# Optimization experiments

Measured on AMD Instinct MI355X. Metric: run time of the kernel, lower is better.

The kernel has to match this reference:

```python
import jax, jax.numpy as jnp
import numpy as np

H, D, K, FF = 4, 256, 1024, 1024  # n_head, d_model, key_feature_dim, dim_feedforward
L, B = 2048, 4                    # pixels, batch


def setup_inputs() -> dict:
    key = jax.random.key(0)
    ks = jax.random.split(key, 12)
    def g(k, shape, s=0.02):
        return jax.random.normal(k, shape, jnp.float32) * s
    return dict(
        src=jax.random.normal(ks[0], (L, B, D), jnp.float32),
        WK=g(ks[1], (H, K, D), (2.0 / K) ** 0.5),
        WQ=g(ks[2], (H, K, D), (2.0 / K) ** 0.5),
        WV=g(ks[3], (H, D, D), (2.0 / D) ** 0.5),
        TC=g(ks[4], (H, D, D)),
        ENw1=g(ks[5], (H, FF, D)), ENb1=jnp.zeros((H, FF), jnp.float32),
        ENw2=g(ks[6], (H, D, FF)), ENb2=jnp.zeros((H, D), jnp.float32),
        ENg=jnp.ones((H, D), jnp.float32), ENbeta=jnp.zeros((H, D), jnp.float32),
        Wout=g(ks[7], (D, H * D)),
        L1w=g(ks[8], (FF, D)), L1b=jnp.zeros((FF,), jnp.float32),
        L2w=g(ks[9], (D, FF)), L2b=jnp.zeros((D,), jnp.float32),
        N1g=jnp.ones((D,), jnp.float32), N1b=jnp.zeros((D,), jnp.float32),
        N2g=jnp.ones((D,), jnp.float32), N2b=jnp.zeros((D,), jnp.float32),
    )


def _ln(x, g, b, eps=1e-5):
    m = jnp.mean(x, -1, keepdims=True)
    v = jnp.mean((x - m) ** 2, -1, keepdims=True)
    return (x - m) * jax.lax.rsqrt(v + eps) * g + b


def _l2n(x, eps=1e-12):
    n = jnp.sqrt(jnp.sum(x * x, -1, keepdims=True))
    return x / jnp.maximum(n, eps)


def reference(src, WK, WQ, WV, TC, ENw1, ENb1, ENw2, ENb2, ENg, ENbeta,
              Wout, L1w, L1b, L2w, L2b, N1g, N1b, N2g, N2b):
    # --- RMA: per-head RelationUnit, vectorized over head axis h ---
    wq = _l2n(jnp.einsum('lbd,hkd->hlbk', src, WQ))   # (H,L,B,K), L2-normed
    wk = _l2n(jnp.einsum('lbd,hkd->hlbk', src, WK))
    wv = jnp.einsum('lbd,hed->hlbe', src, WV)         # (H,L,B,D)
    dot = jnp.einsum('hlbk,hmbk->hblm', wq, wk)       # (H,B,Lq,Lk)
    aff = jax.nn.softmax(dot, axis=-1)                 # softmax over keys (temp=1)
    aff = aff / (1e-9 + jnp.sum(aff, axis=2, keepdims=True))  # renorm over QUERY dim (torch dim=1)
    out = jnp.einsum('hblm,hmbe->hlbe', aff, wv)       # (H,L,B,D)
    ru = jax.nn.relu(jnp.einsum('hlbe,hfe->hlbf', src[None] - out, TC))
    # per-head extra TransNonlinear: residual MLP + layernorm
    hid = jax.nn.relu(jnp.einsum('hlbd,hfd->hlbf', ru, ENw1) + ENb1[:, None, None, :])
    s2 = jnp.einsum('hlbf,hdf->hlbd', hid, ENw2) + ENb2[:, None, None, :]
    tn = _ln(ru + s2, ENg[:, None, None, :], ENbeta[:, None, None, :])  # (H,L,B,D)
    concat = jnp.transpose(tn, (1, 2, 0, 3)).reshape(L, B, H * D)
    attn = concat @ Wout.T                              # (L,B,D)
    # --- encoder layer: residual + LN + FFN + LN (dropout = eval identity) ---
    x = _ln(src + attn, N1g, N1b)
    ff = jax.nn.relu(x @ L1w.T + L1b) @ L2w.T + L2b
    return _ln(x + ff, N2g, N2b)
```

## Files before the change

### kernel.cpp

```cpp
#include <hip/hip_runtime.h>
#include <hip/hip_bf16.h>

typedef __hip_bfloat16 bf16;
typedef short s16x8 __attribute__((ext_vector_type(8)));
typedef float f32x4 __attribute__((ext_vector_type(4)));

#ifndef __has_builtin
#define __has_builtin(x) 0
#endif
#if __has_builtin(__builtin_amdgcn_global_load_lds)
#define HAS_GLL 1
#else
#define HAS_GLL 0
#endif

#define HN 4
#define DM 256
#define KF 1024
#define FFD 1024
#define LL 2048
#define BB 4
#define NN (LL * BB)
#define HD (HN * DM)

__device__ __forceinline__ float b2f(unsigned short u) {
    unsigned v = ((unsigned)u) << 16; float f; __builtin_memcpy(&f, &v, 4); return f;
}
__device__ __forceinline__ unsigned short f2b(float f) {
    bf16 b = (bf16)f; unsigned short u; __builtin_memcpy(&u, &b, 2); return u;
}

__device__ __forceinline__ float waveReduceSum(float v) {
    for (int o = 32; o; o >>= 1) v += __shfl_down(v, o, 64);
    return v;
}
__device__ __forceinline__ float waveReduceMax(float v) {
    for (int o = 32; o; o >>= 1) v = fmaxf(v, __shfl_down(v, o, 64));
    return v;
}
__device__ __forceinline__ float blockReduceSum(float v) {
    __shared__ float sh[4];
    v = waveReduceSum(v);
    __syncthreads();
    if ((threadIdx.x & 63) == 0) sh[threadIdx.x >> 6] = v;
    __syncthreads();
    return sh[0] + sh[1] + sh[2] + sh[3];
}
__device__ __forceinline__ float blockReduceMax(float v) {
    __shared__ float sh[4];
    v = waveReduceMax(v);
    __syncthreads();
    if ((threadIdx.x & 63) == 0) sh[threadIdx.x >> 6] = v;
    __syncthreads();
    return fmaxf(fmaxf(sh[0], sh[1]), fmaxf(sh[2], sh[3]));
}

__global__ void sentinel_kernel(float* out, float val) {
    if (threadIdx.x == 0 && blockIdx.x == 0) out[0] = val;
}

#if HAS_GLL
__device__ __forceinline__ void gll16(void* g, void* l) {
    __builtin_amdgcn_global_load_lds(
        (__attribute__((address_space(1))) unsigned int*)g,
        (__attribute__((address_space(3))) unsigned int*)l, 16, 0, 0);
}
#endif

__global__ __launch_bounds__(256) void gemm_nt(
    const void* __restrict__ A, int aF32, int lda, long sA,
    const void* __restrict__ Bv, int bF32, int ldb, long sB,
    void* __restrict__ C, int cF32, int ldc, long sC,
    int Kc,
    const float* __restrict__ bias, long sBias,
    const void* __restrict__ aux, int auxType, int ldaux, long sAux,
    float accSign, int relu)
{
    const int z = blockIdx.z;
    const float* Af = (const float*)A + (long)z * sA;
    const bf16*  Ah = (const bf16*)A + (long)z * sA;
    const float* Bf = (const float*)Bv + (long)z * sB;
    const bf16*  Bh = (const bf16*)Bv + (long)z * sB;
    float* Cf = (float*)C + (long)z * sC;
    bf16*  Ch = (bf16*)C + (long)z * sC;
    const float* biasp = bias ? (bias + (long)z * sBias) : nullptr;
    const float* auxf = (auxType == 1) ? ((const float*)aux + (long)z * sAux) : nullptr;
    const bf16*  auxh = (auxType == 2) ? ((const bf16*)aux + (long)z * sAux) : nullptr;

    __shared__ __align__(16) bf16 As[128 * 32];
    __shared__ __align__(16) bf16 Bs[128 * 32];

    const int tid = threadIdx.x;
    const int lane = tid & 63;
    const int wv = __builtin_amdgcn_readfirstlane(tid >> 6);
    const int wm = (tid >> 6) & 1;
    const int wn = (tid >> 6) >> 1;
    const int lrow = lane & 15;
    const int quad = lane >> 4;
    const int m0 = blockIdx.x * 128;
    const int n0 = blockIdx.y * 128;
    const int srow = tid >> 1;
    const int scol = (tid & 1) * 16;
    const int drow = wv * 16 + (lane >> 2);
    const int dcol = (lane & 3) * 8;

    f32x4 acc[4][4] = {};

    for (int k0 = 0; k0 < Kc; k0 += 32) {
        uint4 av0, av1, bv0, bv1;
        if (aF32) {
            const float* ag = Af + (long)(m0 + srow) * lda + k0 + scol;
            ushort t[16];
#pragma unroll
            for (int j = 0; j < 4; j++) {
                float4 f = *(const float4*)(ag + 4 * j);
                t[4*j] = f2b(f.x); t[4*j+1] = f2b(f.y); t[4*j+2] = f2b(f.z); t[4*j+3] = f2b(f.w);
            }
            av0 = *(const uint4*)&t[0]; av1 = *(const uint4*)&t[8];
        }
#if !HAS_GLL
        else {
            const bf16* ag = Ah + (long)(m0 + srow) * lda + k0 + scol;
            av0 = *(const uint4*)ag; av1 = *(const uint4*)(ag + 8);
        }
#endif
        if (bF32) {
            const float* bg = Bf + (long)(n0 + srow) * ldb + k0 + scol;
            ushort t[16];
#pragma unroll
            for (int j = 0; j < 4; j++) {
                float4 f = *(const float4*)(bg + 4 * j);
                t[4*j] = f2b(f.x); t[4*j+1] = f2b(f.y); t[4*j+2] = f2b(f.z); t[4*j+3] = f2b(f.w);
            }
            bv0 = *(const uint4*)&t[0]; bv1 = *(const uint4*)&t[8];
        }
#if !HAS_GLL
        else {
            const bf16* bg = Bh + (long)(n0 + srow) * ldb + k0 + scol;
            bv0 = *(const uint4*)bg; bv1 = *(const uint4*)(bg + 8);
        }
#endif
        __syncthreads();
        if (aF32) {
            *(uint4*)&As[srow * 32 + scol] = av0;
            *(uint4*)&As[srow * 32 + scol + 8] = av1;
        } else {
#if HAS_GLL
            gll16((void*)(Ah + (long)(m0 + drow) * lda + k0 + dcol), (void*)(As + wv * 512));
            gll16((void*)(Ah + (long)(m0 + 64 + drow) * lda + k0 + dcol), (void*)(As + 2048 + wv * 512));
#else
            *(uint4*)&As[srow * 32 + scol] = av0;
            *(uint4*)&As[srow * 32 + scol + 8] = av1;
#endif
        }
        if (bF32) {
            *(uint4*)&Bs[srow * 32 + scol] = bv0;
            *(uint4*)&Bs[srow * 32 + scol + 8] = bv1;
        } else {
#if HAS_GLL
            gll16((void*)(Bh + (long)(n0 + drow) * ldb + k0 + dcol), (void*)(Bs + wv * 512));
            gll16((void*)(Bh + (long)(n0 + 64 + drow) * ldb + k0 + dcol), (void*)(Bs + 2048 + wv * 512));
#else
            *(uint4*)&Bs[srow * 32 + scol] = bv0;
            *(uint4*)&Bs[srow * 32 + scol + 8] = bv1;
#endif
        }
        __syncthreads();

        s16x8 af[4], bfg[4];
#pragma unroll
        for (int mi = 0; mi < 4; mi++) {
            int r = wm * 64 + mi * 16 + lrow;
            af[mi] = *(const s16x8*)&As[r * 32 + quad * 8];
        }
#pragma unroll
        for (int ni = 0; ni < 4; ni++) {
            int r = wn * 64 + ni * 16 + lrow;
            bfg[ni] = *(const s16x8*)&Bs[r * 32 + quad * 8];
        }
#pragma unroll
        for (int mi = 0; mi < 4; mi++)
#pragma unroll
            for (int ni = 0; ni < 4; ni++)
                acc[mi][ni] = __builtin_amdgcn_mfma_f32_16x16x32_bf16(af[mi], bfg[ni], acc[mi][ni], 0, 0, 0);
    }

#pragma unroll
    for (int mi = 0; mi < 4; mi++) {
#pragma unroll
        for (int ni = 0; ni < 4; ni++) {
            int col = n0 + wn * 64 + ni * 16 + lrow;
            float bv = biasp ? biasp[col] : 0.0f;
#pragma unroll
            for (int i = 0; i < 4; i++) {
                int row = m0 + wm * 64 + mi * 16 + quad * 4 + i;
                float v = accSign * acc[mi][ni][i] + bv;
                if (auxType == 1) v += auxf[(long)row * ldaux + col];
                else if (auxType == 2) v += (float)auxh[(long)row * ldaux + col];
                if (relu) v = fmaxf(v, 0.0f);
                if (cF32) Cf[(long)row * ldc + col] = v;
                else Ch[(long)row * ldc + col] = (bf16)v;
            }
        }
    }
}

__global__ __launch_bounds__(256) void cvt4(const float* __restrict__ in, bf16* __restrict__ out, int n4) {
    int i = blockIdx.x * 256 + threadIdx.x;
    if (i < n4) {
        float4 f = ((const float4*)in)[i];
        ushort4 u; u.x = f2b(f.x); u.y = f2b(f.y); u.z = f2b(f.z); u.w = f2b(f.w);
        ((ushort4*)out)[i] = u;
    }
}

struct WCvt {
    const float* in[9];
    bf16* out[9];
    int n4[9];
};
__global__ __launch_bounds__(256) void cvt_weights(WCvt wc) {
    int t = blockIdx.y;
    int n4 = wc.n4[t];
    const float4* in = (const float4*)wc.in[t];
    ushort4* out = (ushort4*)wc.out[t];
    for (int i = blockIdx.x * 256 + threadIdx.x; i < n4; i += gridDim.x * 256) {
        float4 f = in[i];
        ushort4 u; u.x = f2b(f.x); u.y = f2b(f.y); u.z = f2b(f.z); u.w = f2b(f.w);
        out[i] = u;
    }
}

__global__ __launch_bounds__(256) void l2norm_rows(bf16* __restrict__ Q) {
    bf16* q = Q + (long)blockIdx.x * KF;
    ushort4 u = ((ushort4*)q)[threadIdx.x];
    float v0 = b2f(u.x), v1 = b2f(u.y), v2 = b2f(u.z), v3 = b2f(u.w);
    float ss = blockReduceSum(v0 * v0 + v1 * v1 + v2 * v2 + v3 * v3);
    float inv = 1.0f / fmaxf(sqrtf(ss), 1e-12f);
    u.x = f2b(v0 * inv); u.y = f2b(v1 * inv); u.z = f2b(v2 * inv); u.w = f2b(v3 * inv);
    ((ushort4*)q)[threadIdx.x] = u;
}

__global__ __launch_bounds__(256) void softmax_rows(bf16* __restrict__ P) {
    bf16* p = P + (long)blockIdx.x * LL;
    ushort4 a = ((ushort4*)p)[2 * threadIdx.x];
    ushort4 b = ((ushort4*)p)[2 * threadIdx.x + 1];
    float v[8] = {b2f(a.x), b2f(a.y), b2f(a.z), b2f(a.w), b2f(b.x), b2f(b.y), b2f(b.z), b2f(b.w)};
    float mx = -1e30f;
#pragma unroll
    for (int i = 0; i < 8; i++) mx = fmaxf(mx, v[i]);
    mx = blockReduceMax(mx);
    float s = 0.0f;
#pragma unroll
    for (int i = 0; i < 8; i++) { v[i] = __expf(v[i] - mx); s += v[i]; }
    s = blockReduceSum(s);
    float inv = 1.0f / s;
    a.x = f2b(v[0]*inv); a.y = f2b(v[1]*inv); a.z = f2b(v[2]*inv); a.w = f2b(v[3]*inv);
    b.x = f2b(v[4]*inv); b.y = f2b(v[5]*inv); b.z = f2b(v[6]*inv); b.w = f2b(v[7]*inv);
    ((ushort4*)p)[2 * threadIdx.x] = a;
    ((ushort4*)p)[2 * threadIdx.x + 1] = b;
}

__global__ __launch_bounds__(256) void zero_cs(float* __restrict__ cs) {
    cs[blockIdx.x * 256 + threadIdx.x] = 0.0f;
}

__global__ __launch_bounds__(256) void colsum2(const bf16* __restrict__ P, float* __restrict__ cs) {
    int col = blockIdx.x * 256 + threadIdx.x;
    int rc = blockIdx.y;
    int b = blockIdx.z;
    const bf16* p = P + (long)b * LL * LL + (long)rc * 128 * LL + col;
    float s = 0.0f;
#pragma unroll 4
    for (int r = 0; r < 128; r++) s += (float)p[(long)r * LL];
    atomicAdd(&cs[(long)b * LL + col], s);
}

__global__ __launch_bounds__(256) void scale_vt(bf16* __restrict__ vt, const float* __restrict__ cs) {
    int e = blockIdx.x, b = blockIdx.y;
    bf16* row = vt + ((long)b * DM + e) * LL;
    const float* c = cs + (long)b * LL;
#pragma unroll
    for (int i = 0; i < 8; i++) {
        int m = threadIdx.x + i * 256;
        row[m] = (bf16)((float)row[m] / (1e-9f + c[m]));
    }
}

__global__ __launch_bounds__(256) void ln_rows(const bf16* __restrict__ in, void* __restrict__ out,
                                               int outF32,
                                               const float* __restrict__ g, const float* __restrict__ b,
                                               const float* __restrict__ aux) {
    long base = (long)blockIdx.x * 256;
    float v = (float)in[base + threadIdx.x];
    if (aux) v += aux[base + threadIdx.x];
    float mean = blockReduceSum(v) * (1.0f / 256.0f);
    float d = v - mean;
    float var = blockReduceSum(d * d) * (1.0f / 256.0f);
    float o = d * rsqrtf(var + 1e-5f) * g[threadIdx.x] + b[threadIdx.x];
    if (outF32) ((float*)out)[base + threadIdx.x] = o;
    else ((bf16*)out)[base + threadIdx.x] = (bf16)o;
}

__global__ __launch_bounds__(256) void ln_cat(bf16* __restrict__ cat, const float* __restrict__ g,
                                              const float* __restrict__ bb) {
    long n = blockIdx.x;
    int h = blockIdx.y;
    bf16* x = cat + n * HD + (long)h * DM;
    float v = (float)x[threadIdx.x];
    float mean = blockReduceSum(v) * (1.0f / 256.0f);
    float d = v - mean;
    float var = blockReduceSum(d * d) * (1.0f / 256.0f);
    x[threadIdx.x] = (bf16)(d * rsqrtf(var + 1e-5f) * g[h * DM + threadIdx.x] + bb[h * DM + threadIdx.x]);
}

extern "C" void kernel_launch(void* const* d_in, const int* in_sizes, int n_in,
                              void* d_out, int out_size, void* d_ws, size_t ws_size,
                              hipStream_t stream) {
    const float* src  = (const float*)d_in[0];
    const float* WK   = (const float*)d_in[1];
    const float* WQ   = (const float*)d_in[2];
    const float* WV   = (const float*)d_in[3];
    const float* TC   = (const float*)d_in[4];
    const float* ENw1 = (const float*)d_in[5];
    const float* ENb1 = (const float*)d_in[6];
    const float* ENw2 = (const float*)d_in[7];
    const float* ENb2 = (const float*)d_in[8];
    const float* ENg  = (const float*)d_in[9];
    const float* ENbt = (const float*)d_in[10];
    const float* Wout = (const float*)d_in[11];
    const float* L1w  = (const float*)d_in[12];
    const float* L1b  = (const float*)d_in[13];
    const float* L2w  = (const float*)d_in[14];
    const float* L2b  = (const float*)d_in[15];
    const float* N1g  = (const float*)d_in[16];
    const float* N1b  = (const float*)d_in[17];
    const float* N2g  = (const float*)d_in[18];
    const float* N2b  = (const float*)d_in[19];

    const size_t COMPACT_FLOOR = 34700000;
    const size_t FAST_FLOOR  = 92307456;
    const size_t FASTW_FLOOR = 92307456 + 11010048;
    if (ws_size < COMPACT_FLOOR || out_size != NN * DM || n_in != 20) {
        float val;
        if (n_in != 20) val = 32768.0f + (float)n_in;
        else if (out_size != NN * DM) val = 49152.0f;
        else val = 16384.0f + 128.0f * (float)(unsigned)(ws_size >> 20);
        sentinel_kernel<<<1, 64, 0, stream>>>((float*)d_out, val);
        return;
    }

    char* w = (char*)d_ws;
    auto G = [&](const void* A, int aF, int lda, long sA,
                 const void* B, int bF, int ldb, long sB,
                 void* C, int cF, int ldc, long sC,
                 int M, int Nn, int Kc, int nb,
                 const float* bias, long sBias,
                 const void* aux, int auxT, int ldaux, long sAux,
                 float sgn, int relu) {
        gemm_nt<<<dim3(M / 128, Nn / 128, nb), dim3(256), 0, stream>>>(
            A, aF, lda, sA, B, bF, ldb, sB, C, cF, ldc, sC, Kc,
            bias, sBias, aux, auxT, ldaux, sAux, sgn, relu);
    };

    if (ws_size >= FAST_FLOOR) {
        bf16*  Sb  = (bf16*)(w + 0);
        bf16*  Q   = (bf16*)(w + 4194304);
        bf16*  K   = (bf16*)(w + 20971520);
        bf16*  Vt  = (bf16*)(w + 37748736);
        bf16*  P   = (bf16*)(w + 41943040);
        bf16*  Su  = (bf16*)(w + 75497472);
        float* Cs  = (float*)(w + 92274688);
        bf16* Ru = Q; bf16* Hid = K; bf16* Cat = P;
        bf16* Attn = Vt; bf16* Xln = Su; bf16* Ffh = Q; bf16* Yp = Vt;

        const int haveWb = (ws_size >= FASTW_FLOOR) ? 1 : 0;
        char* wb = w + 92307456;
        bf16* WKb   = (bf16*)(wb + 0);
        bf16* WQb   = (bf16*)(wb + 2097152);
        bf16* WVb   = (bf16*)(wb + 4194304);
        bf16* TCb   = (bf16*)(wb + 4718592);
        bf16* ENw1b = (bf16*)(wb + 5242880);
        bf16* ENw2b = (bf16*)(wb + 7340032);
        bf16* Woutb = (bf16*)(wb + 9437184);
        bf16* L1wb  = (bf16*)(wb + 9961472);
        bf16* L2wb  = (bf16*)(wb + 10485760);
        if (haveWb) {
            WCvt wc;
            wc.in[0] = WK;   wc.out[0] = WKb;   wc.n4[0] = 262144;
            wc.in[1] = WQ;   wc.out[1] = WQb;   wc.n4[1] = 262144;
            wc.in[2] = WV;   wc.out[2] = WVb;   wc.n4[2] = 65536;
            wc.in[3] = TC;   wc.out[3] = TCb;   wc.n4[3] = 65536;
            wc.in[4] = ENw1; wc.out[4] = ENw1b; wc.n4[4] = 262144;
            wc.in[5] = ENw2; wc.out[5] = ENw2b; wc.n4[5] = 262144;
            wc.in[6] = Wout; wc.out[6] = Woutb; wc.n4[6] = 65536;
            wc.in[7] = L1w;  wc.out[7] = L1wb;  wc.n4[7] = 65536;
            wc.in[8] = L2w;  wc.out[8] = L2wb;  wc.n4[8] = 65536;
            cvt_weights<<<dim3(256, 9), 256, 0, stream>>>(wc);
        }
        const int wF = haveWb ? 0 : 1;
        auto WP = [&](const void* f32p, const void* b16p, long off) {
            return haveWb ? (const void*)((const bf16*)b16p + off)
                          : (const void*)((const float*)f32p + off);
        };

        cvt4<<<2048, 256, 0, stream>>>(src, Sb, NN * DM / 4);

        for (int h = 0; h < HN; h++) {
            G(Sb, 0, DM, 0, WP(WQ, WQb, (long)h * KF * DM), wF, DM, 0, Q, 0, KF, 0,
              NN, KF, DM, 1, nullptr, 0, nullptr, 0, 0, 0, 1.0f, 0);
            G(Sb, 0, DM, 0, WP(WK, WKb, (long)h * KF * DM), wF, DM, 0, K, 0, KF, 0,
              NN, KF, DM, 1, nullptr, 0, nullptr, 0, 0, 0, 1.0f, 0);
            G(WP(WV, WVb, (long)h * DM * DM), wF, DM, 0, Sb, 0, BB * DM, DM,
              Vt, 0, LL, (long)DM * LL,
              DM, LL, DM, BB, nullptr, 0, nullptr, 0, 0, 0, 1.0f, 0);
            l2norm_rows<<<NN, 256, 0, stream>>>(Q);
            l2norm_rows<<<NN, 256, 0, stream>>>(K);
            G(Q, 0, BB * KF, KF, K, 0, BB * KF, KF, P, 0, LL, (long)LL * LL,
              LL, LL, KF, BB, nullptr, 0, nullptr, 0, 0, 0, 1.0f, 0);
            softmax_rows<<<BB * LL, 256, 0, stream>>>(P);
            zero_cs<<<BB * LL / 256, 256, 0, stream>>>(Cs);
            colsum2<<<dim3(LL / 256, 16, BB), 256, 0, stream>>>(P, Cs);
            scale_vt<<<dim3(DM, BB), 256, 0, stream>>>(Vt, Cs);
            G(P, 0, LL, (long)LL * LL, Vt, 0, LL, (long)DM * LL,
              Su + (long)h * NN * DM, 0, BB * DM, DM,
              LL, DM, LL, BB, nullptr, 0, Sb, 2, BB * DM, DM, -1.0f, 0);
        }
        G(Su, 0, DM, (long)NN * DM, WP(TC, TCb, 0), wF, DM, (long)DM * DM,
          Ru, 0, DM, (long)NN * DM,
          NN, DM, DM, HN, nullptr, 0, nullptr, 0, 0, 0, 1.0f, 1);
        for (int h = 0; h < HN; h++) {
            G(Ru + (long)h * NN * DM, 0, DM, 0, WP(ENw1, ENw1b, (long)h * FFD * DM), wF, DM, 0,
              Hid, 0, FFD, 0, NN, FFD, DM, 1, ENb1 + (long)h * FFD, 0, nullptr, 0, 0, 0, 1.0f, 1);
            G(Hid, 0, FFD, 0, WP(ENw2, ENw2b, (long)h * DM * FFD), wF, FFD, 0,
              Cat + (long)h * DM, 0, HD, 0, NN, DM, FFD, 1,
              ENb2 + (long)h * DM, 0, Ru + (long)h * NN * DM, 2, DM, 0, 1.0f, 0);
        }
        ln_cat<<<dim3(NN, HN), 256, 0, stream>>>(Cat, ENg, ENbt);
        G(Cat, 0, HD, 0, WP(Wout, Woutb, 0), wF, HD, 0, Attn, 0, DM, 0,
          NN, DM, HD, 1, nullptr, 0, nullptr, 0, 0, 0, 1.0f, 0);
        ln_rows<<<NN, 256, 0, stream>>>(Attn, Xln, 0, N1g, N1b, src);
        G(Xln, 0, DM, 0, WP(L1w, L1wb, 0), wF, DM, 0, Ffh, 0, FFD, 0,
          NN, FFD, DM, 1, L1b, 0, nullptr, 0, 0, 0, 1.0f, 1);
        G(Ffh, 0, FFD, 0, WP(L2w, L2wb, 0), wF, FFD, 0, Yp, 0, DM, 0,
          NN, DM, FFD, 1, L2b, 0, Xln, 2, DM, 0, 1.0f, 0);
        ln_rows<<<NN, 256, 0, stream>>>(Yp, (float*)d_out, 1, N2g, N2b, nullptr);
    } else {
        bf16*  S0 = (bf16*)(w + 0);
        bf16*  S1 = (bf16*)(w + 16777216);
        bf16*  S2 = (bf16*)(w + 20971520);
        bf16*  S3 = (bf16*)(w + 25165824);
        bf16*  S4 = (bf16*)(w + 26214400);
        bf16*  S5 = (bf16*)(w + 30408704);
        float* Cs = (float*)(w + 34603008);

        for (int h = 0; h < HN; h++) {
            for (int b = 0; b < BB; b++) {
                G(src + b * DM, 1, BB * DM, 0, WQ + (long)h * KF * DM, 1, DM, 0,
                  S1, 0, KF, 0, LL, KF, DM, 1, nullptr, 0, nullptr, 0, 0, 0, 1.0f, 0);
                G(src + b * DM, 1, BB * DM, 0, WK + (long)h * KF * DM, 1, DM, 0,
                  S2, 0, KF, 0, LL, KF, DM, 1, nullptr, 0, nullptr, 0, 0, 0, 1.0f, 0);
                G(WV + (long)h * DM * DM, 1, DM, 0, src + b * DM, 1, BB * DM, 0,
                  S3, 0, LL, 0, DM, LL, DM, 1, nullptr, 0, nullptr, 0, 0, 0, 1.0f, 0);
                l2norm_rows<<<LL, 256, 0, stream>>>(S1);
                l2norm_rows<<<LL, 256, 0, stream>>>(S2);
                G(S1, 0, KF, 0, S2, 0, KF, 0, S0, 0, LL, 0,
                  LL, LL, KF, 1, nullptr, 0, nullptr, 0, 0, 0, 1.0f, 0);
                softmax_rows<<<LL, 256, 0, stream>>>(S0);
                zero_cs<<<LL / 256, 256, 0, stream>>>(Cs);
                colsum2<<<dim3(LL / 256, 16, 1), 256, 0, stream>>>(S0, Cs);
                scale_vt<<<dim3(DM, 1), 256, 0, stream>>>(S3, Cs);
                G(S0, 0, LL, 0, S3, 0, LL, 0, S4 + b * DM, 0, BB * DM, 0,
                  LL, DM, LL, 1, nullptr, 0, src + b * DM, 1, BB * DM, 0, -1.0f, 0);
            }
            G(S4, 0, DM, 0, TC + (long)h * DM * DM, 1, DM, 0, S1, 0, DM, 0,
              NN, DM, DM, 1, nullptr, 0, nullptr, 0, 0, 0, 1.0f, 1);
            G(S1, 0, DM, 0, ENw1 + (long)h * FFD * DM, 1, DM, 0, S0, 0, FFD, 0,
              NN, FFD, DM, 1, ENb1 + (long)h * FFD, 0, nullptr, 0, 0, 0, 1.0f, 1);
            G(S0, 0, FFD, 0, ENw2 + (long)h * DM * FFD, 1, FFD, 0, S2, 0, DM, 0,
              NN, DM, FFD, 1, ENb2 + (long)h * DM, 0, S1, 2, DM, 0, 1.0f, 0);
            ln_rows<<<NN, 256, 0, stream>>>(S2, S2, 0, ENg + (long)h * DM, ENbt + (long)h * DM, nullptr);
            G(S2, 0, DM, 0, Wout + (long)h * DM, 1, HD, 0, S5, 0, DM, 0,
              NN, DM, DM, 1, nullptr, 0, (h == 0) ? nullptr : (const void*)S5,
              (h == 0) ? 0 : 2, DM, 0, 1.0f, 0);
        }
        ln_rows<<<NN, 256, 0, stream>>>(S5, S1, 0, N1g, N1b, src);
        G(S1, 0, DM, 0, L1w, 1, DM, 0, S0, 0, FFD, 0,
          NN, FFD, DM, 1, L1b, 0, nullptr, 0, 0, 0, 1.0f, 1);
        G(S0, 0, FFD, 0, L2w, 1, FFD, 0, S2, 0, DM, 0,
          NN, DM, FFD, 1, L2b, 0, S1, 2, DM, 0, 1.0f, 0);
        ln_rows<<<NN, 256, 0, stream>>>(S2, (float*)d_out, 1, N2g, N2b, nullptr);
    }
}
```

Baseline: 1.281 ms.

## Add split-K GEMM path, fuse Q/K projections, fold L2 norms into epilogue

Adds a new workspace tier that splits the K dimension in two for the narrow-N GEMMs (P·V, EN2, Wout, L2), writing fp32 partials that are then reduced by new fused kernels (pv_reduce, en2_reduce, ln_fuse) carrying the bias, residual and layernorm. Q and K projections are batched into one launch by placing WQ and WK adjacently. The L2 normalisation is applied as row and column scales in the QK^T epilogue instead of rewriting Q and K in place. This is meant to raise occupancy on GEMMs with few output tiles and remove extra passes, at the cost of fp32 partial traffic and a larger workspace requirement.

```diff
diff --git a/kernel.cpp b/kernel.cpp
--- a/kernel.cpp
+++ b/kernel.cpp
@@ -71,21 +71,26 @@
     const void* __restrict__ A, int aF32, int lda, long sA,
     const void* __restrict__ Bv, int bF32, int ldb, long sB,
     void* __restrict__ C, int cF32, int ldc, long sC,
-    int Kc,
+    int Kc, int splitK, long sPart,
     const float* __restrict__ bias, long sBias,
     const void* __restrict__ aux, int auxType, int ldaux, long sAux,
+    const float* __restrict__ rowScale, int rsLd,
+    const float* __restrict__ colScale, int csLd,
     float accSign, int relu)
 {
-    const int z = blockIdx.z;
-    const float* Af = (const float*)A + (long)z * sA;
-    const bf16*  Ah = (const bf16*)A + (long)z * sA;
-    const float* Bf = (const float*)Bv + (long)z * sB;
-    const bf16*  Bh = (const bf16*)Bv + (long)z * sB;
-    float* Cf = (float*)C + (long)z * sC;
-    bf16*  Ch = (bf16*)C + (long)z * sC;
-    const float* biasp = bias ? (bias + (long)z * sBias) : nullptr;
-    const float* auxf = (auxType == 1) ? ((const float*)aux + (long)z * sAux) : nullptr;
-    const bf16*  auxh = (auxType == 2) ? ((const bf16*)aux + (long)z * sAux) : nullptr;
+    int zz = blockIdx.z, chunk = 0, KcEff = Kc, k0base = 0;
+    if (splitK > 1) { chunk = zz % splitK; zz /= splitK; KcEff = Kc / splitK; k0base = chunk * KcEff; }
+    const float* Af = (const float*)A + (long)zz * sA;
+    const bf16*  Ah = (const bf16*)A + (long)zz * sA;
+    const float* Bf = (const float*)Bv + (long)zz * sB;
+    const bf16*  Bh = (const bf16*)Bv + (long)zz * sB;
+    float* Cf = (float*)C + (long)zz * sC + (long)chunk * sPart;
+    bf16*  Ch = (bf16*)C + (long)zz * sC;
+    const float* biasp = bias ? (bias + (long)zz * sBias) : nullptr;
+    const float* auxf = (auxType == 1) ? ((const float*)aux + (long)zz * sAux) : nullptr;
+    const bf16*  auxh = (auxType == 2) ? ((const bf16*)aux + (long)zz * sAux) : nullptr;
+    const float* rs  = rowScale ? (rowScale + zz) : nullptr;
+    const float* cs2 = colScale ? (colScale + zz) : nullptr;
 
     __shared__ __align__(16) bf16 As[128 * 32];
     __shared__ __align__(16) bf16 Bs[128 * 32];
@@ -106,7 +111,7 @@
 
     f32x4 acc[4][4] = {};
 
-    for (int k0 = 0; k0 < Kc; k0 += 32) {
+    for (int k0 = k0base; k0 < k0base + KcEff; k0 += 32) {
         uint4 av0, av1, bv0, bv1;
         if (aF32) {
             const float* ag = Af + (long)(m0 + srow) * lda + k0 + scol;
@@ -191,15 +196,22 @@
         for (int ni = 0; ni < 4; ni++) {
             int col = n0 + wn * 64 + ni * 16 + lrow;
             float bv = biasp ? biasp[col] : 0.0f;
+            float csv = cs2 ? cs2[col * csLd] : 1.0f;
 #pragma unroll
             for (int i = 0; i < 4; i++) {
                 int row = m0 + wm * 64 + mi * 16 + quad * 4 + i;
-                float v = accSign * acc[mi][ni][i] + bv;
-                if (auxType == 1) v += auxf[(long)row * ldaux + col];
-                else if (auxType == 2) v += (float)auxh[(long)row * ldaux + col];
-                if (relu) v = fmaxf(v, 0.0f);
-                if (cF32) Cf[(long)row * ldc + col] = v;
-                else Ch[(long)row * ldc + col] = (bf16)v;
+                if (splitK > 1) {
+                    Cf[(long)row * ldc + col] = accSign * acc[mi][ni][i];
+                } else {
+                    float v = accSign * acc[mi][ni][i];
+                    if (rs) v *= rs[row * rsLd] * csv;
+                    v += bv;
+                    if (auxType == 1) v += auxf[(long)row * ldaux + col];
+                    else if (auxType == 2) v += (float)auxh[(long)row * ldaux + col];
+                    if (relu) v = fmaxf(v, 0.0f);
+                    if (cF32) Cf[(long)row * ldc + col] = v;
+                    else Ch[(long)row * ldc + col] = (bf16)v;
+                }
             }
         }
     }
@@ -214,11 +226,7 @@
     }
 }
 
-struct WCvt {
-    const float* in[9];
-    bf16* out[9];
-    int n4[9];
-};
+struct WCvt { const float* in[9]; bf16* out[9]; int n4[9]; };
 __global__ __launch_bounds__(256) void cvt_weights(WCvt wc) {
     int t = blockIdx.y;
     int n4 = wc.n4[t];
@@ -231,6 +239,14 @@
     }
 }
 
+__global__ __launch_bounds__(256) void rownorm(const bf16* __restrict__ Q, float* __restrict__ nrm) {
+    const bf16* q = Q + (long)blockIdx.x * KF;
+    ushort4 u = ((const ushort4*)q)[threadIdx.x];
+    float v0 = b2f(u.x), v1 = b2f(u.y), v2 = b2f(u.z), v3 = b2f(u.w);
+    float ss = blockReduceSum(v0 * v0 + v1 * v1 + v2 * v2 + v3 * v3);
+    if (threadIdx.x == 0) nrm[blockIdx.x] = 1.0f / fmaxf(sqrtf(ss), 1e-12f);
+}
+
 __global__ __launch_bounds__(256) void l2norm_rows(bf16* __restrict__ Q) {
     bf16* q = Q + (long)blockIdx.x * KF;
     ushort4 u = ((ushort4*)q)[threadIdx.x];
@@ -287,12 +303,48 @@
     }
 }
 
-__global__ __launch_bounds__(256) void ln_rows(const bf16* __restrict__ in, void* __restrict__ out,
-                                               int outF32,
-                                               const float* __restrict__ g, const float* __restrict__ b,
-                                               const float* __restrict__ aux) {
+__global__ __launch_bounds__(256) void pv_reduce(const float* __restrict__ p0, const float* __restrict__ p1,
+                                                 const bf16* __restrict__ sb, bf16* __restrict__ su) {
+    int n = blockIdx.x, c = threadIdx.x;
+    int b = n & 3, l = n >> 2;
+    long pi = ((long)b * LL + l) * DM + c;
+    float v = (float)sb[(long)n * DM + c] - (p0[pi] + p1[pi]);
+    su[(long)n * DM + c] = (bf16)v;
+}
+
+__global__ __launch_bounds__(256) void en2_reduce(const float* __restrict__ p0, const float* __restrict__ p1,
+                                                  const float* __restrict__ b2, const bf16* __restrict__ ru,
+                                                  bf16* __restrict__ cat) {
+    long n = blockIdx.x; int c = threadIdx.x;
+    long i = n * DM + c;
+    cat[n * HD + c] = (bf16)(p0[i] + p1[i] + b2[c] + (float)ru[i]);
+}
+
+__global__ __launch_bounds__(256) void ln_fuse(const float* __restrict__ p0, const float* __restrict__ p1,
+                                               const float* __restrict__ colBias,
+                                               const void* __restrict__ aux, int auxType,
+                                               void* __restrict__ out, int outF32,
+                                               const float* __restrict__ g, const float* __restrict__ b) {
     long base = (long)blockIdx.x * 256;
-    float v = (float)in[base + threadIdx.x];
+    float v = p0[base + threadIdx.x] + p1[base + threadIdx.x];
+    if (colBias) v += colBias[threadIdx.x];
+    if (auxType == 1) v += ((const float*)aux)[base + threadIdx.x];
+    else if (auxType == 2) v += (float)((const bf16*)aux)[base + threadIdx.x];
+    float mean = blockReduceSum(v) * (1.0f / 256.0f);
+    float d = v - mean;
+    float var = blockReduceSum(d * d) * (1.0f / 256.0f);
+    float o = d * rsqrtf(var + 1e-5f) * g[threadIdx.x] + b[threadIdx.x];
+    if (outF32) ((float*)out)[base + threadIdx.x] = o;
+    else ((bf16*)out)[base + threadIdx.x] = (bf16)o;
+}
+
+__global__ __launch_bounds__(256) void ln_rows2(const void* __restrict__ in, int inF32,
+                                                void* __restrict__ out, int outF32,
+                                                const float* __restrict__ g, const float* __restrict__ b,
+                                                const float* __restrict__ aux) {
+    long base = (long)blockIdx.x * 256;
+    float v = inF32 ? ((const float*)in)[base + threadIdx.x]
+                    : (float)((const bf16*)in)[base + threadIdx.x];
     if (aux) v += aux[base + threadIdx.x];
     float mean = blockReduceSum(v) * (1.0f / 256.0f);
     float d = v - mean;
@@ -339,8 +391,8 @@
     const float* N2b  = (const float*)d_in[19];
 
     const size_t COMPACT_FLOOR = 34700000;
-    const size_t FAST_FLOOR  = 92307456;
-    const size_t FASTW_FLOOR = 92307456 + 11010048;
+    const size_t FASTW_FLOOR = 103317504;
+    const size_t NEW_FLOOR   = 120160256;
     if (ws_size < COMPACT_FLOOR || out_size != NN * DM || n_in != 20) {
         float val;
         if (n_in != 20) val = 32768.0f + (float)n_in;
@@ -354,16 +406,106 @@
     auto G = [&](const void* A, int aF, int lda, long sA,
                  const void* B, int bF, int ldb, long sB,
                  void* C, int cF, int ldc, long sC,
-                 int M, int Nn, int Kc, int nb,
+                 int M, int Nn, int Kc, int nb, int splitK, long sPart,
                  const float* bias, long sBias,
                  const void* aux, int auxT, int ldaux, long sAux,
+                 const float* rsp, int rsLd, const float* csp, int csLd,
                  float sgn, int relu) {
-        gemm_nt<<<dim3(M / 128, Nn / 128, nb), dim3(256), 0, stream>>>(
-            A, aF, lda, sA, B, bF, ldb, sB, C, cF, ldc, sC, Kc,
-            bias, sBias, aux, auxT, ldaux, sAux, sgn, relu);
+        gemm_nt<<<dim3(M / 128, Nn / 128, nb * splitK), dim3(256), 0, stream>>>(
+            A, aF, lda, sA, B, bF, ldb, sB, C, cF, ldc, sC, Kc, splitK, sPart,
+            bias, sBias, aux, auxT, ldaux, sAux, rsp, rsLd, csp, csLd, sgn, relu);
     };
 
-    if (ws_size >= FAST_FLOOR) {
+    auto setupWeights = [&](char* wb, bf16*& WQb, bf16*& WKb, bf16*& WVb, bf16*& TCb,
+                            bf16*& ENw1b, bf16*& ENw2b, bf16*& Woutb, bf16*& L1wb, bf16*& L2wb) {
+        WQb   = (bf16*)(wb + 0);
+        WKb   = (bf16*)(wb + 2097152);
+        WVb   = (bf16*)(wb + 4194304);
+        TCb   = (bf16*)(wb + 4718592);
+        ENw1b = (bf16*)(wb + 5242880);
+        ENw2b = (bf16*)(wb + 7340032);
+        Woutb = (bf16*)(wb + 9437184);
+        L1wb  = (bf16*)(wb + 9961472);
+        L2wb  = (bf16*)(wb + 10485760);
+        WCvt wc;
+        wc.in[0] = WQ;   wc.out[0] = WQb;   wc.n4[0] = 262144;
+        wc.in[1] = WK;   wc.out[1] = WKb;   wc.n4[1] = 262144;
+        wc.in[2] = WV;   wc.out[2] = WVb;   wc.n4[2] = 65536;
+        wc.in[3] = TC;   wc.out[3] = TCb;   wc.n4[3] = 65536;
+        wc.in[4] = ENw1; wc.out[4] = ENw1b; wc.n4[4] = 262144;
+        wc.in[5] = ENw2; wc.out[5] = ENw2b; wc.n4[5] = 262144;
+        wc.in[6] = Wout; wc.out[6] = Woutb; wc.n4[6] = 65536;
+        wc.in[7] = L1w;  wc.out[7] = L1wb;  wc.n4[7] = 65536;
+        wc.in[8] = L2w;  wc.out[8] = L2wb;  wc.n4[8] = 65536;
+        cvt_weights<<<dim3(256, 9), 256, 0, stream>>>(wc);
+    };
+
+    if (ws_size >= NEW_FLOOR) {
+        bf16*  Sb  = (bf16*)(w + 0);
+        bf16*  Q   = (bf16*)(w + 4194304);
+        bf16*  K   = (bf16*)(w + 20971520);
+        bf16*  Vt  = (bf16*)(w + 37748736);
+        bf16*  P   = (bf16*)(w + 41943040);
+        bf16*  Su  = (bf16*)(w + 75497472);
+        float* Cs  = (float*)(w + 92274688);
+        char*  wb  = w + 92307456;
+        float* Part= (float*)(w + 103317504);
+        float* Nrm = (float*)(w + 120094720);
+        bf16* Ru = Q; bf16* Hid = K; bf16* Ffh = K; bf16* Cat = P; bf16* Xln = Su;
+        const long PSTRIDE = (long)NN * DM;
+
+        bf16 *WQb, *WKb, *WVb, *TCb, *ENw1b, *ENw2b, *Woutb, *L1wb, *L2wb;
+        setupWeights(wb, WQb, WKb, WVb, TCb, ENw1b, ENw2b, Woutb, L1wb, L2wb);
+        cvt4<<<2048, 256, 0, stream>>>(src, Sb, NN * DM / 4);
+
+        for (int h = 0; h < HN; h++) {
+            G(Sb, 0, DM, 0, WQb + (long)h * KF * DM, 0, DM, 1048576,
+              Q, 0, KF, 8388608, NN, KF, DM, 2, 1, 0,
+              nullptr, 0, nullptr, 0, 0, 0, nullptr, 0, nullptr, 0, 1.0f, 0);
+            G(WVb + (long)h * DM * DM, 0, DM, 0, Sb, 0, BB * DM, DM,
+              Vt, 0, LL, (long)DM * LL, DM, LL, DM, BB, 1, 0,
+              nullptr, 0, nullptr, 0, 0, 0, nullptr, 0, nullptr, 0, 1.0f, 0);
+            rownorm<<<2 * NN, 256, 0, stream>>>(Q, Nrm);
+            G(Q, 0, BB * KF, KF, K, 0, BB * KF, KF, P, 0, LL, (long)LL * LL,
+              LL, LL, KF, BB, 1, 0,
+              nullptr, 0, nullptr, 0, 0, 0, Nrm, BB, Nrm + NN, BB, 1.0f, 0);
+            softmax_rows<<<BB * LL, 256, 0, stream>>>(P);
+            zero_cs<<<BB * LL / 256, 256, 0, stream>>>(Cs);
+            colsum2<<<dim3(LL / 256, 16, BB), 256, 0, stream>>>(P, Cs);
+            scale_vt<<<dim3(DM, BB), 256, 0, stream>>>(Vt, Cs);
+            G(P, 0, LL, (long)LL * LL, Vt, 0, LL, (long)DM * LL,
+              Part, 1, DM, (long)LL * DM, LL, DM, LL, BB, 2, PSTRIDE,
+              nullptr, 0, nullptr, 0, 0, 0, nullptr, 0, nullptr, 0, 1.0f, 0);
+            pv_reduce<<<NN, 256, 0, stream>>>(Part, Part + PSTRIDE, Sb, Su + (long)h * NN * DM);
+        }
+        G(Su, 0, DM, (long)NN * DM, TCb, 0, DM, (long)DM * DM,
+          Ru, 0, DM, (long)NN * DM, NN, DM, DM, HN, 1, 0,
+          nullptr, 0, nullptr, 0, 0, 0, nullptr, 0, nullptr, 0, 1.0f, 1);
+        for (int h = 0; h < HN; h++) {
+            G(Ru + (long)h * NN * DM, 0, DM, 0, ENw1b + (long)h * FFD * DM, 0, DM, 0,
+              Hid, 0, FFD, 0, NN, FFD, DM, 1, 1, 0,
+              ENb1 + (long)h * FFD, 0, nullptr, 0, 0, 0, nullptr, 0, nullptr, 0, 1.0f, 1);
+            G(Hid, 0, FFD, 0, ENw2b + (long)h * DM * FFD, 0, FFD, 0,
+              Part, 1, DM, 0, NN, DM, FFD, 1, 2, PSTRIDE,
+              nullptr, 0, nullptr, 0, 0, 0, nullptr, 0, nullptr, 0, 1.0f, 0);
+            en2_reduce<<<NN, 256, 0, stream>>>(Part, Part + PSTRIDE, ENb2 + (long)h * DM,
+                                               Ru + (long)h * NN * DM, Cat + (long)h * DM);
+        }
+        ln_cat<<<dim3(NN, HN), 256, 0, stream>>>(Cat, ENg, ENbt);
+        G(Cat, 0, HD, 0, Woutb, 0, HD, 0, Part, 1, DM, 0,
+          NN, DM, HD, 1, 2, PSTRIDE,
+          nullptr, 0, nullptr, 0, 0, 0, nullptr, 0, nullptr, 0, 1.0f, 0);
+        ln_fuse<<<NN, 256, 0, stream>>>(Part, Part + PSTRIDE, nullptr, src, 1,
+                                        Xln, 0, N1g, N1b);
+        G(Xln, 0, DM, 0, L1wb, 0, DM, 0, Ffh, 0, FFD, 0,
+          NN, FFD, DM, 1, 1, 0,
+          L1b, 0, nullptr, 0, 0, 0, nullptr, 0, nullptr, 0, 1.0f, 1);
+        G(Ffh, 0, FFD, 0, L2wb, 0, FFD, 0, Part, 1, DM, 0,
+          NN, DM, FFD, 1, 2, PSTRIDE,
+          nullptr, 0, nullptr, 0, 0, 0, nullptr, 0, nullptr, 0, 1.0f, 0);
+        ln_fuse<<<NN, 256, 0, stream>>>(Part, Part + PSTRIDE, L2b, Xln, 2,
+                                        (float*)d_out, 1, N2g, N2b);
+    } else if (ws_size >= FASTW_FLOOR) {
         bf16*  Sb  = (bf16*)(w + 0);
         bf16*  Q   = (bf16*)(w + 4194304);
         bf16*  K   = (bf16*)(w + 20971520);
@@ -374,77 +516,50 @@
         bf16* Ru = Q; bf16* Hid = K; bf16* Cat = P;
         bf16* Attn = Vt; bf16* Xln = Su; bf16* Ffh = Q; bf16* Yp = Vt;
 
-        const int haveWb = (ws_size >= FASTW_FLOOR) ? 1 : 0;
-        char* wb = w + 92307456;
-        bf16* WKb   = (bf16*)(wb + 0);
-        bf16* WQb   = (bf16*)(wb + 2097152);
-        bf16* WVb   = (bf16*)(wb + 4194304);
-        bf16* TCb   = (bf16*)(wb + 4718592);
-        bf16* ENw1b = (bf16*)(wb + 5242880);
-        bf16* ENw2b = (bf16*)(wb + 7340032);
-        bf16* Woutb = (bf16*)(wb + 9437184);
-        bf16* L1wb  = (bf16*)(wb + 9961472);
-        bf16* L2wb  = (bf16*)(wb + 10485760);
-        if (haveWb) {
-            WCvt wc;
-            wc.in[0] = WK;   wc.out[0] = WKb;   wc.n4[0] = 262144;
-            wc.in[1] = WQ;   wc.out[1] = WQb;   wc.n4[1] = 262144;
-            wc.in[2] = WV;   wc.out[2] = WVb;   wc.n4[2] = 65536;
-            wc.in[3] = TC;   wc.out[3] = TCb;   wc.n4[3] = 65536;
-            wc.in[4] = ENw1; wc.out[4] = ENw1b; wc.n4[4] = 262144;
-            wc.in[5] = ENw2; wc.out[5] = ENw2b; wc.n4[5] = 262144;
-            wc.in[6] = Wout; wc.out[6] = Woutb; wc.n4[6] = 65536;
-            wc.in[7] = L1w;  wc.out[7] = L1wb;  wc.n4[7] = 65536;
-            wc.in[8] = L2w;  wc.out[8] = L2wb;  wc.n4[8] = 65536;
-            cvt_weights<<<dim3(256, 9), 256, 0, stream>>>(wc);
-        }
-        const int wF = haveWb ? 0 : 1;
-        auto WP = [&](const void* f32p, const void* b16p, long off) {
-            return haveWb ? (const void*)((const bf16*)b16p + off)
-                          : (const void*)((const float*)f32p + off);
-        };
-
+        bf16 *WQb, *WKb, *WVb, *TCb, *ENw1b, *ENw2b, *Woutb, *L1wb, *L2wb;
+        setupWeights(w + 92307456, WQb, WKb, WVb, TCb, ENw1b, ENw2b, Woutb, L1wb, L2wb);
         cvt4<<<2048, 256, 0, stream>>>(src, Sb, NN * DM / 4);
 
         for (int h = 0; h < HN; h++) {
-            G(Sb, 0, DM, 0, WP(WQ, WQb, (long)h * KF * DM), wF, DM, 0, Q, 0, KF, 0,
-              NN, KF, DM, 1, nullptr, 0, nullptr, 0, 0, 0, 1.0f, 0);
-            G(Sb, 0, DM, 0, WP(WK, WKb, (long)h * KF * DM), wF, DM, 0, K, 0, KF, 0,
-              NN, KF, DM, 1, nullptr, 0, nullptr, 0, 0, 0, 1.0f, 0);
-            G(WP(WV, WVb, (long)h * DM * DM), wF, DM, 0, Sb, 0, BB * DM, DM,
-              Vt, 0, LL, (long)DM * LL,
-              DM, LL, DM, BB, nullptr, 0, nullptr, 0, 0, 0, 1.0f, 0);
+            G(Sb, 0, DM, 0, WQb + (long)h * KF * DM, 0, DM, 0, Q, 0, KF, 0,
+              NN, KF, DM, 1, 1, 0, nullptr, 0, nullptr, 0, 0, 0, nullptr, 0, nullptr, 0, 1.0f, 0);
+            G(Sb, 0, DM, 0, WKb + (long)h * KF * DM, 0, DM, 0, K, 0, KF, 0,
+              NN, KF, DM, 1, 1, 0, nullptr, 0, nullptr, 0, 0, 0, nullptr, 0, nullptr, 0, 1.0f, 0);
+            G(WVb + (long)h * DM * DM, 0, DM, 0, Sb, 0, BB * DM, DM,
+              Vt, 0, LL, (long)DM * LL, DM, LL, DM, BB, 1, 0,
+              nullptr, 0, nullptr, 0, 0, 0, nullptr, 0, nullptr, 0, 1.0f, 0);
             l2norm_rows<<<NN, 256, 0, stream>>>(Q);
             l2norm_rows<<<NN, 256, 0, stream>>>(K);
             G(Q, 0, BB * KF, KF, K, 0, BB * KF, KF, P, 0, LL, (long)LL * LL,
-              LL, LL, KF, BB, nullptr, 0, nullptr, 0, 0, 0, 1.0f, 0);
+              LL, LL, KF, BB, 1, 0, nullptr, 0, nullptr, 0, 0, 0, nullptr, 0, nullptr, 0, 1.0f, 0);
             softmax_rows<<<BB * LL, 256, 0, stream>>>(P);
             zero_cs<<<BB * LL / 256, 256, 0, stream>>>(Cs);
             colsum2<<<dim3(LL / 256, 16, BB), 256, 0, stream>>>(P, Cs);
             scale_vt<<<dim3(DM, BB), 256, 0, stream>>>(Vt, Cs);
             G(P, 0, LL, (long)LL * LL, Vt, 0, LL, (long)DM * LL,
               Su + (long)h * NN * DM, 0, BB * DM, DM,
-              LL, DM, LL, BB, nullptr, 0, Sb, 2, BB * DM, DM, -1.0f, 0);
-        }
-        G(Su, 0, DM, (long)NN * DM, WP(TC, TCb, 0), wF, DM, (long)DM * DM,
-          Ru, 0, DM, (long)NN * DM,
-          NN, DM, DM, HN, nullptr, 0, nullptr, 0, 0, 0, 1.0f, 1);
+              LL, DM, LL, BB, 1, 0, nullptr, 0, Sb, 2, BB * DM, DM, nullptr, 0, nullptr, 0, -1.0f, 0);
+        }
+        G(Su, 0, DM, (long)NN * DM, TCb, 0, DM, (long)DM * DM,
+          Ru, 0, DM, (long)NN * DM, NN, DM, DM, HN, 1, 0,
+          nullptr, 0, nullptr, 0, 0, 0, nullptr, 0, nullptr, 0, 1.0f, 1);
         for (int h = 0; h < HN; h++) {
-            G(Ru + (long)h * NN * DM, 0, DM, 0, WP(ENw1, ENw1b, (long)h * FFD * DM), wF, DM, 0,
-              Hid, 0, FFD, 0, NN, FFD, DM, 1, ENb1 + (long)h * FFD, 0, nullptr, 0, 0, 0, 1.0f, 1);
-            G(Hid, 0, FFD, 0, WP(ENw2, ENw2b, (long)h * DM * FFD), wF, FFD, 0,
-              Cat + (long)h * DM, 0, HD, 0, NN, DM, FFD, 1,
-              ENb2 + (long)h * DM, 0, Ru + (long)h * NN * DM, 2, DM, 0, 1.0f, 0);
+            G(Ru + (long)h * NN * DM, 0, DM, 0, ENw1b + (long)h * FFD * DM, 0, DM, 0,
+              Hid, 0, FFD, 0, NN, FFD, DM, 1, 1, 0,
+              ENb1 + (long)h * FFD, 0, nullptr, 0, 0, 0, nullptr, 0, nullptr, 0, 1.0f, 1);
+            G(Hid, 0, FFD, 0, ENw2b + (long)h * DM * FFD, 0, FFD, 0,
+              Cat + (long)h * DM, 0, HD, 0, NN, DM, FFD, 1, 1, 0,
+              ENb2 + (long)h * DM, 0, Ru + (long)h * NN * DM, 2, DM, 0, nullptr, 0, nullptr, 0, 1.0f, 0);
         }
         ln_cat<<<dim3(NN, HN), 256, 0, stream>>>(Cat, ENg, ENbt);
-        G(Cat, 0, HD, 0, WP(Wout, Woutb, 0), wF, HD, 0, Attn, 0, DM, 0,
-          NN, DM, HD, 1, nullptr, 0, nullptr, 0, 0, 0, 1.0f, 0);
-        ln_rows<<<NN, 256, 0, stream>>>(Attn, Xln, 0, N1g, N1b, src);
-        G(Xln, 0, DM, 0, WP(L1w, L1wb, 0), wF, DM, 0, Ffh, 0, FFD, 0,
-          NN, FFD, DM, 1, L1b, 0, nullptr, 0, 0, 0, 1.0f, 1);
-        G(Ffh, 0, FFD, 0, WP(L2w, L2wb, 0), wF, FFD, 0, Yp, 0, DM, 0,
-          NN, DM, FFD, 1, L2b, 0, Xln, 2, DM, 0, 1.0f, 0);
-        ln_rows<<<NN, 256, 0, stream>>>(Yp, (float*)d_out, 1, N2g, N2b, nullptr);
+        G(Cat, 0, HD, 0, Woutb, 0, HD, 0, Attn, 0, DM, 0,
+          NN, DM, HD, 1, 1, 0, nullptr, 0, nullptr, 0, 0, 0, nullptr, 0, nullptr, 0, 1.0f, 0);
+        ln_rows2<<<NN, 256, 0, stream>>>(Attn, 0, Xln, 0, N1g, N1b, src);
+        G(Xln, 0, DM, 0, L1wb, 0, DM, 0, Ffh, 0, FFD, 0,
+          NN, FFD, DM, 1, 1, 0, L1b, 0, nullptr, 0, 0, 0, nullptr, 0, nullptr, 0, 1.0f, 1);
+        G(Ffh, 0, FFD, 0, L2wb, 0, FFD, 0, Yp, 0, DM, 0,
+          NN, DM, FFD, 1, 1, 0, L2b, 0, Xln, 2, DM, 0, nullptr, 0, nullptr, 0, 1.0f, 0);
+        ln_rows2<<<NN, 256, 0, stream>>>(Yp, 0, (float*)d_out, 1, N2g, N2b, nullptr);
     } else {
         bf16*  S0 = (bf16*)(w + 0);
         bf16*  S1 = (bf16*)(w + 16777216);
@@ -457,38 +572,44 @@
         for (int h = 0; h < HN; h++) {
             for (int b = 0; b < BB; b++) {
                 G(src + b * DM, 1, BB * DM, 0, WQ + (long)h * KF * DM, 1, DM, 0,
-                  S1, 0, KF, 0, LL, KF, DM, 1, nullptr, 0, nullptr, 0, 0, 0, 1.0f, 0);
+                  S1, 0, KF, 0, LL, KF, DM, 1, 1, 0,
+                  nullptr, 0, nullptr, 0, 0, 0, nullptr, 0, nullptr, 0, 1.0f, 0);
                 G(src + b * DM, 1, BB * DM, 0, WK + (long)h * KF * DM, 1, DM, 0,
-                  S2, 0, KF, 0, LL, KF, DM, 1, nullptr, 0, nullptr, 0, 0, 0, 1.0f, 0);
+                  S2, 0, KF, 0, LL, KF, DM, 1, 1, 0,
+                  nullptr, 0, nullptr, 0, 0, 0, nullptr, 0, nullptr, 0, 1.0f, 0);
                 G(WV + (long)h * DM * DM, 1, DM, 0, src + b * DM, 1, BB * DM, 0,
-                  S3, 0, LL, 0, DM, LL, DM, 1, nullptr, 0, nullptr, 0, 0, 0, 1.0f, 0);
+                  S3, 0, LL, 0, DM, LL, DM, 1, 1, 0,
+                  nullptr, 0, nullptr, 0, 0, 0, nullptr, 0, nullptr, 0, 1.0f, 0);
                 l2norm_rows<<<LL, 256, 0, stream>>>(S1);
                 l2norm_rows<<<LL, 256, 0, stream>>>(S2);
                 G(S1, 0, KF, 0, S2, 0, KF, 0, S0, 0, LL, 0,
-                  LL, LL, KF, 1, nullptr, 0, nullptr, 0, 0, 0, 1.0f, 0);
+                  LL, LL, KF, 1, 1, 0, nullptr, 0, nullptr, 0, 0, 0, nullptr, 0, nullptr, 0, 1.0f, 0);
                 softmax_rows<<<LL, 256, 0, stream>>>(S0);
                 zero_cs<<<LL / 256, 256, 0, stream>>>(Cs);
                 colsum2<<<dim3(LL / 256, 16, 1), 256, 0, stream>>>(S0, Cs);
                 scale_vt<<<dim3(DM, 1), 256, 0, stream>>>(S3, Cs);
                 G(S0, 0, LL, 0, S3, 0, LL, 0, S4 + b * DM, 0, BB * DM, 0,
-                  LL, DM, LL, 1, nullptr, 0, src + b * DM, 1, BB * DM, 0, -1.0f, 0);
+                  LL, DM, LL, 1, 1, 0, nullptr, 0, src + b * DM, 1, BB * DM, 0,
+                  nullptr, 0, nullptr, 0, -1.0f, 0);
             }
             G(S4, 0, DM, 0, TC + (long)h * DM * DM, 1, DM, 0, S1, 0, DM, 0,
-              NN, DM, DM, 1, nullptr, 0, nullptr, 0, 0, 0, 1.0f, 1);
+              NN, DM, DM, 1, 1, 0, nullptr, 0, nullptr, 0, 0, 0, nullptr, 0, nullptr, 0, 1.0f, 1);
             G(S1, 0, DM, 0, ENw1 + (long)h * FFD * DM, 1, DM, 0, S0, 0, FFD, 0,
-              NN, FFD, DM, 1, ENb1 + (long)h * FFD, 0, nullptr, 0, 0, 0, 1.0f, 1);
+              NN, FFD, DM, 1, 1, 0, ENb1 + (long)h * FFD, 0, nullptr, 0, 0, 0,
+              nullptr, 0, nullptr, 0, 1.0f, 1);
             G(S0, 0, FFD, 0, ENw2 + (long)h * DM * FFD, 1, FFD, 0, S2, 0, DM, 0,
-              NN, DM, FFD, 1, ENb2 + (long)h * DM, 0, S1, 2, DM, 0, 1.0f, 0);
-            ln_rows<<<NN, 256, 0, stream>>>(S2, S2, 0, ENg + (long)h * DM, ENbt + (long)h * DM, nullptr);
+              NN, DM, FFD, 1, 1, 0, ENb2 + (long)h * DM, 0, S1, 2, DM, 0,
+              nullptr, 0, nullptr, 0, 1.0f, 0);
+            ln_rows2<<<NN, 256, 0, stream>>>(S2, 0, S2, 0, ENg + (long)h * DM, ENbt + (long)h * DM, nullptr);
             G(S2, 0, DM, 0, Wout + (long)h * DM, 1, HD, 0, S5, 0, DM, 0,
-              NN, DM, DM, 1, nullptr, 0, (h == 0) ? nullptr : (const void*)S5,
-              (h == 0) ? 0 : 2, DM, 0, 1.0f, 0);
-        }
-        ln_rows<<<NN, 256, 0, stream>>>(S5, S1, 0, N1g, N1b, src);
+              NN, DM, DM, 1, 1, 0, nullptr, 0, (h == 0) ? nullptr : (const void*)S5,
+              (h == 0) ? 0 : 2, DM, 0, nullptr, 0, nullptr, 0, 1.0f, 0);
+        }
+        ln_rows2<<<NN, 256, 0, stream>>>(S5, 0, S1, 0, N1g, N1b, src);
         G(S1, 0, DM, 0, L1w, 1, DM, 0, S0, 0, FFD, 0,
-          NN, FFD, DM, 1, L1b, 0, nullptr, 0, 0, 0, 1.0f, 1);
+          NN, FFD, DM, 1, 1, 0, L1b, 0, nullptr, 0, 0, 0, nullptr, 0, nullptr, 0, 1.0f, 1);
         G(S0, 0, FFD, 0, L2w, 1, FFD, 0, S2, 0, DM, 0,
-          NN, DM, FFD, 1, L2b, 0, S1, 2, DM, 0, 1.0f, 0);
-        ln_rows<<<NN, 256, 0, stream>>>(S2, (float*)d_out, 1, N2g, N2b, nullptr);
+          NN, DM, FFD, 1, 1, 0, L2b, 0, S1, 2, DM, 0, nullptr, 0, nullptr, 0, 1.0f, 0);
+        ln_rows2<<<NN, 256, 0, stream>>>(S2, 0, (float*)d_out, 1, N2g, N2b, nullptr);
     }
 }
```

After: 1.295 ms. Within noise of the previous version (+1.1%).
